# Kernel optimization log

Measured on AMD Instinct MI355X. Metric: run time of the kernel, lower is better.

Reference implementation:

```python
import jax, jax.numpy as jnp
import numpy as np

B, K, U, P, H, L, TD = 512, 1024, 16, 32, 128, 32, 64
THETA_LO, THETA_HI = 1e-3, 2.0


def _glorot(key, shape):
    fan = shape[0] + shape[1]
    lim = np.sqrt(6.0 / fan).astype(np.float32)
    return jax.random.uniform(key, shape, jnp.float32, -lim, lim)


def setup_inputs() -> dict:
    key = jax.random.key(0)
    ks = jax.random.split(key, 12)
    return {
        "y0": jax.random.normal(ks[0], (B, P), jnp.float32),
        "u_seq": jax.random.normal(ks[1], (B, K, U), jnp.float32),
        "dt_seq": jax.random.uniform(ks[2], (B, K), jnp.float32),
        "y_seq": jax.random.normal(ks[3], (B, K, P), jnp.float32),
        "u_to_y_jump": _glorot(ks[4], (U, P)),
        "lift_W": _glorot(ks[5], (L, U + P)),
        "lift_b": jnp.zeros((L,), jnp.float32),
        "w_ih": _glorot(ks[6], (3 * H, L)),
        "w_hh": _glorot(ks[7], (3 * H, H)),
        "b_ih": jnp.zeros((3 * H,), jnp.float32),
        "b_hh": jnp.zeros((3 * H,), jnp.float32),
        "head_W": _glorot(ks[8], (TD, H)),
        "head_b": jnp.zeros((TD,), jnp.float32),
        "tf_every": 50,
    }


def _rk4_step(y, h_dt, theta):
    # scaffold: linear ODE f(y) = -a*y + b, a=theta[:, :P], b=theta[:, P:]
    a, b = theta[:, :P], theta[:, P:]
    f = lambda yy: -a * yy + b
    k1 = f(y)
    k2 = f(y + 0.5 * h_dt * k1)
    k3 = f(y + 0.5 * h_dt * k2)
    k4 = f(y + h_dt * k3)
    return y + (h_dt / 6.0) * (k1 + 2.0 * k2 + 2.0 * k3 + k4)


def _forward(y0, u_seq, dt_seq, y_seq, u_to_y_jump, lift_W, lift_b,
             w_ih, w_hh, b_ih, b_hh, head_W, head_b, tf_every):
    k_idx = jnp.arange(K)
    use_tf = (k_idx > 0) & (k_idx % tf_every == 0)            # (K,)
    y_tf = jnp.concatenate([y_seq[:, :1], y_seq[:, :-1]], 1)  # y_seq[:, k-1]
    xs = (jnp.swapaxes(u_seq, 0, 1),                 # (K,B,U)
          jnp.swapaxes(dt_seq, 0, 1)[..., None],     # (K,B,1)
          jnp.swapaxes(y_tf, 0, 1),                  # (K,B,P)
          use_tf)

    def step(carry, xk):
        y_prev, h = carry
        u_k, dt_k, ytf_k, tf_k = xk
        y_in = jax.lax.stop_gradient(jnp.where(tf_k, ytf_k, y_prev))
        feat = jnp.concatenate([u_k, y_in], -1)               # (B, U+P)
        x = jax.nn.silu(feat @ lift_W.T + lift_b)             # (B, L)
        gi = x @ w_ih.T + b_ih                                # (B, 3H)
        gh = h @ w_hh.T + b_hh                                # (B, 3H)
        i_r, i_z, i_n = jnp.split(gi, 3, -1)
        h_r, h_z, h_n = jnp.split(gh, 3, -1)
        r = jax.nn.sigmoid(i_r + h_r)
        zg = jax.nn.sigmoid(i_z + h_z)
        n = jnp.tanh(i_n + r * h_n)
        h_new = (1.0 - zg) * n + zg * h                       # PyTorch GRU update
        raw = h_new @ head_W.T + head_b
        theta = THETA_LO + (THETA_HI - THETA_LO) * jax.nn.sigmoid(raw)
        y = y_prev + u_k @ u_to_y_jump                        # input jump
        y = _rk4_step(y, dt_k, theta)                         # n_substeps = 1
        return (y, h_new), (y, theta)

    h0 = jnp.zeros((y0.shape[0], H), u_seq.dtype)
    _, (ys, ths) = jax.lax.scan(step, (y0, h0), xs)
    return jnp.swapaxes(ys, 0, 1), jnp.swapaxes(ths, 0, 1)   # (B,K,P), (B,K,TD)


def reference(y0, u_seq, dt_seq, y_seq, u_to_y_jump, lift_W, lift_b,
              w_ih, w_hh, b_ih, b_hh, head_W, head_b, tf_every):
    return _forward(y0, u_seq, dt_seq, y_seq, u_to_y_jump, lift_W, lift_b,
                    w_ih, w_hh, b_ih, b_hh, head_W, head_b, tf_every)
```

## Files before the change

kernel.cpp:

```cpp
#include <hip/hip_runtime.h>
#include <math.h>


typedef float v2f __attribute__((ext_vector_type(2)));

__device__ __forceinline__ v2f mkv2(float a, float b) {
  v2f r; r.x = a; r.y = b; return r;
}

#define PKD4(acc2, v, w2, pb)                                             \
  acc2 = __builtin_elementwise_fma(mkv2((v).x, (v).y), (w2)[(pb)], acc2); \
  acc2 = __builtin_elementwise_fma(mkv2((v).z, (v).w), (w2)[(pb) + 1], acc2);

__device__ __forceinline__ float sigf(float x) {
  return 1.0f / (1.0f + __expf(-x));
}

__device__ __forceinline__ float tanh_fast(float x) {
  float ax = fabsf(x);
  float e = __expf(2.0f * ax);
  float r = 1.0f - 2.0f / (e + 1.0f);
  return copysignf(r, x);
}

template <int CTRL>
__device__ __forceinline__ float dpp_add(float x) {
  int s = __float_as_int(x);
  int r = __builtin_amdgcn_update_dpp(s, s, CTRL, 0xF, 0xF, false);
  return x + __int_as_float(r);
}

#define HP(c) ((c) + 4 * ((c) >> 5))
#define HROW 144

extern "C" __global__ __launch_bounds__(512, 2) void odernn_kernel(
    const float* __restrict__ y0, const float* __restrict__ u_seq,
    const float* __restrict__ dt_seq, const float* __restrict__ y_seq,
    const float* __restrict__ u2y, const float* __restrict__ lift_W,
    const float* __restrict__ lift_b, const float* __restrict__ w_ih,
    const float* __restrict__ w_hh, const float* __restrict__ b_ih,
    const float* __restrict__ b_hh, const float* __restrict__ head_W,
    const float* __restrict__ head_b, const int* __restrict__ tf_p,
    float* __restrict__ out_ys, float* __restrict__ out_th) {
  __shared__ __align__(16) float hbufP[2][2][HROW];
  __shared__ __align__(16) float xL[2][32];
  __shared__ __align__(16) float featL[2][48];
  __shared__ float thetaL[2][64];
  __shared__ float dtL[2];
  __shared__ float liftL[32 * 49];
  __shared__ float u2yL[512];

  const int t = threadIdx.x;
  const int b0 = blockIdx.x * 2;
  const int j = t >> 2;
  const int qj = t & 3;
  const int ho = t >> 3;
  const int he = t & 7;
  const int tfe = *tf_p;

  v2f wr2[20], wz2[20], wn2[20];
  {
    const int jr = j, jz = j + 128, jn = j + 256;
#pragma unroll
    for (int cc = 0; cc < 8; ++cc) {
      const int c = 8 * qj + cc;
      wr2[cc >> 1][cc & 1] = w_ih[jr * 32 + c];
      wz2[cc >> 1][cc & 1] = w_ih[jz * 32 + c];
      wn2[cc >> 1][cc & 1] = w_ih[jn * 32 + c];
    }
#pragma unroll
    for (int cc = 0; cc < 32; ++cc) {
      const int c = 32 * qj + cc;
      wr2[4 + (cc >> 1)][cc & 1] = w_hh[jr * 128 + c];
      wz2[4 + (cc >> 1)][cc & 1] = w_hh[jz * 128 + c];
      wn2[4 + (cc >> 1)][cc & 1] = w_hh[jn * 128 + c];
    }
  }
  v2f wh2[8];
#pragma unroll
  for (int i = 0; i < 16; ++i)
    wh2[i >> 1][i & 1] = head_W[ho * 128 + 16 * he + i];

  const float bR = b_ih[j] + b_hh[j];
  const float bZ = b_ih[j + 128] + b_hh[j + 128];
  const float bIn = b_ih[j + 256];
  const float bHn = b_hh[j + 256];
  const float hb = head_b[ho];
  const float lb = lift_b[t & 31];

  for (int idx = t; idx < 32 * 48; idx += 512)
    liftL[(idx / 48) * 49 + (idx % 48)] = lift_W[idx];
  u2yL[t] = u2y[t];
  for (int idx = t; idx < 2 * 2 * HROW; idx += 512)
    (&hbufP[0][0][0])[idx] = 0.0f;

  float hreg[2] = {0.0f, 0.0f};
  float yreg = 0.0f;
  float upf = 0.0f, dtpf = 0.0f;
  if (t < 64) yreg = y0[(b0 + (t >> 5)) * 32 + (t & 31)];

  __syncthreads();

  if (t < 64) {
    const int bb = t >> 5, jj = t & 31;
    if (t < 32)
      featL[t >> 4][t & 15] =
          u_seq[((size_t)(b0 + (t >> 4)) * 1024 + 0) * 16 + (t & 15)];
    if (t >= 32 && t < 34) dtL[t - 32] = dt_seq[(size_t)(b0 + t - 32) * 1024];
    featL[bb][16 + jj] = yreg;
    if (t < 32)
      upf = u_seq[((size_t)(b0 + (t >> 4)) * 1024 + 1) * 16 + (t & 15)];
    if (t >= 32 && t < 34) dtpf = dt_seq[(size_t)(b0 + t - 32) * 1024 + 1];
    v2f a2 = {0.f, 0.f};
#pragma unroll
    for (int i = 0; i < 48; i += 2)
      a2 = __builtin_elementwise_fma(
          mkv2(featL[bb][i], featL[bb][i + 1]),
          mkv2(liftL[jj * 49 + i], liftL[jj * 49 + i + 1]), a2);
    float acc = a2.x + a2.y + lb;
    xL[bb][jj] = acc * sigf(acc);
  }
  int mtfk = 0;
  __syncthreads();

  for (int k = 0; k < 1024; ++k) {
    const int rp = k & 1;

#pragma unroll
    for (int bb = 0; bb < 2; ++bb) {
      v2f aR2 = {0.f, 0.f}, aZ2 = {0.f, 0.f};
      v2f aI2 = {0.f, 0.f}, aN2 = {0.f, 0.f};
      const float4* xv = reinterpret_cast<const float4*>(&xL[bb][8 * qj]);
      {
        float4 v = xv[0];
        PKD4(aR2, v, wr2, 0) PKD4(aZ2, v, wz2, 0) PKD4(aI2, v, wn2, 0)
        v = xv[1];
        PKD4(aR2, v, wr2, 2) PKD4(aZ2, v, wz2, 2) PKD4(aI2, v, wn2, 2)
      }
      const float4* hv =
          reinterpret_cast<const float4*>(&hbufP[rp][bb][36 * qj]);
#pragma unroll
      for (int i = 0; i < 8; ++i) {
        float4 v = hv[i];
        PKD4(aR2, v, wr2, 4 + 2 * i)
        PKD4(aZ2, v, wz2, 4 + 2 * i)
        PKD4(aN2, v, wn2, 4 + 2 * i)
      }
      float aR = aR2.x + aR2.y;
      float aZ = aZ2.x + aZ2.y;
      float aI = aI2.x + aI2.y;
      float aN = aN2.x + aN2.y;
      aR = dpp_add<0xB1>(aR); aR = dpp_add<0x4E>(aR);
      aZ = dpp_add<0xB1>(aZ); aZ = dpp_add<0x4E>(aZ);
      aI = dpp_add<0xB1>(aI); aI = dpp_add<0x4E>(aI);
      aN = dpp_add<0xB1>(aN); aN = dpp_add<0x4E>(aN);
      float r = sigf(aR + bR);
      float z = sigf(aZ + bZ);
      float n = tanh_fast(aI + bIn + r * (aN + bHn));
      float hn = (1.0f - z) * n + z * hreg[bb];
      hreg[bb] = hn;
      if (qj == 0) hbufP[rp ^ 1][bb][HP(j)] = hn;
    }
    __syncthreads();

    {
      float s[2];
#pragma unroll
      for (int bb = 0; bb < 2; ++bb) {
        const float4* h4 =
            reinterpret_cast<const float4*>(&hbufP[rp ^ 1][bb][HP(16 * he)]);
        v2f a2 = {0.f, 0.f};
#pragma unroll
        for (int i = 0; i < 4; ++i) {
          float4 v = h4[i];
          PKD4(a2, v, wh2, 2 * i)
        }
        float a = a2.x + a2.y;
        a = dpp_add<0xB1>(a); a = dpp_add<0x4E>(a); a = dpp_add<0x104>(a);
        s[bb] = a;
      }
      if (he == 0) {
#pragma unroll
        for (int bb = 0; bb < 2; ++bb) {
          float th = 0.001f + 1.999f * sigf(s[bb] + hb);
          thetaL[bb][ho] = th;
          out_th[((size_t)(b0 + bb) * 1024 + k) * 64 + ho] = th;
        }
      }
    }
    __syncthreads();

    if (t < 64) {
      const int bb = t >> 5, jj = t & 31;
      v2f y2 = {0.f, 0.f};
#pragma unroll
      for (int i = 0; i < 16; i += 2)
        y2 = __builtin_elementwise_fma(
            mkv2(featL[bb][i], featL[bb][i + 1]),
            mkv2(u2yL[i * 32 + jj], u2yL[(i + 1) * 32 + jj]), y2);
      float y = yreg + y2.x + y2.y;
      float a = thetaL[bb][jj];
      float b2 = thetaL[bb][32 + jj];
      float hdt = dtL[bb];
      float k1 = b2 - a * y;
      float k2 = b2 - a * (y + 0.5f * hdt * k1);
      float k3 = b2 - a * (y + 0.5f * hdt * k2);
      float k4 = b2 - a * (y + hdt * k3);
      y += hdt * (1.0f / 6.0f) * (k1 + 2.0f * k2 + 2.0f * k3 + k4);
      yreg = y;
      out_ys[((size_t)(b0 + bb) * 1024 + k) * 32 + jj] = y;
      if (t < 32) featL[t >> 4][t & 15] = upf;
      if (t >= 32 && t < 34) dtL[t - 32] = dtpf;
      {
        const int kn = (k + 2 < 1024) ? k + 2 : 1023;
        if (t < 32)
          upf = u_seq[((size_t)(b0 + (t >> 4)) * 1024 + kn) * 16 + (t & 15)];
        if (t >= 32 && t < 34)
          dtpf = dt_seq[(size_t)(b0 + t - 32) * 1024 + kn];
      }
      float yin = y;
      if (mtfk == tfe - 1)
        yin = y_seq[((size_t)(b0 + bb) * 1024 + k) * 32 + jj];
      featL[bb][16 + jj] = yin;
      v2f a2 = {0.f, 0.f};
#pragma unroll
      for (int i = 0; i < 48; i += 2)
        a2 = __builtin_elementwise_fma(
            mkv2(featL[bb][i], featL[bb][i + 1]),
            mkv2(liftL[jj * 49 + i], liftL[jj * 49 + i + 1]), a2);
      float acc = a2.x + a2.y + lb;
      xL[bb][jj] = acc * sigf(acc);
    }
    mtfk = (mtfk + 1 == tfe) ? 0 : mtfk + 1;
    __syncthreads();
  }
}

extern "C" void kernel_launch(void* const* d_in, const int* in_sizes, int n_in,
                              void* d_out, int out_size, void* d_ws,
                              size_t ws_size, hipStream_t stream) {
  (void)in_sizes; (void)n_in; (void)out_size; (void)d_ws; (void)ws_size;
  const float* y0     = (const float*)d_in[0];
  const float* u_seq  = (const float*)d_in[1];
  const float* dt_seq = (const float*)d_in[2];
  const float* y_seq  = (const float*)d_in[3];
  const float* u2y    = (const float*)d_in[4];
  const float* lift_W = (const float*)d_in[5];
  const float* lift_b = (const float*)d_in[6];
  const float* w_ih   = (const float*)d_in[7];
  const float* w_hh   = (const float*)d_in[8];
  const float* b_ih   = (const float*)d_in[9];
  const float* b_hh   = (const float*)d_in[10];
  const float* head_W = (const float*)d_in[11];
  const float* head_b = (const float*)d_in[12];
  const int*   tf_p   = (const int*)d_in[13];

  float* out_ys = (float*)d_out;
  float* out_th = out_ys + (size_t)512 * 1024 * 32;

  odernn_kernel<<<dim3(256), dim3(512), 0, stream>>>(
      y0, u_seq, dt_seq, y_seq, u2y, lift_W, lift_b, w_ih, w_hh, b_ih, b_hh,
      head_W, head_b, tf_p, out_ys, out_th);
}
```

Baseline: 2.751 ms.

## Replicate lift/RK4 stage per wavefront to drop a block barrier per step

Every wavefront now redundantly computes the input jump, RK4 update and lift MLP into its own private shared-memory copies of feat, x and dt. Each wave reads only its own copy in the next GRU step, so the third block-wide barrier per timestep is removed. The remaining barriers use a hand-rolled s_waitcnt lgkmcnt(0) plus s_barrier instead of __syncthreads. The cost is eight times the work on this small stage and more redundant global prefetch loads, in exchange for one fewer full-block sync on the serial critical path.

Measured after the change: 3.049 ms. 1.11x slower.

```diff
diff --git a/kernel.cpp b/kernel.cpp
--- a/kernel.cpp
+++ b/kernel.cpp
@@ -29,6 +29,13 @@
   int r = __builtin_amdgcn_update_dpp(s, s, CTRL, 0xF, 0xF, false);
   return x + __int_as_float(r);
 }
+
+#define BAR()                                            \
+  do {                                                   \
+    asm volatile("s_waitcnt lgkmcnt(0)" ::: "memory");   \
+    __builtin_amdgcn_s_barrier();                        \
+    asm volatile("" ::: "memory");                       \
+  } while (0)
 
 #define HP(c) ((c) + 4 * ((c) >> 5))
 #define HROW 144
@@ -43,14 +50,16 @@
     const float* __restrict__ head_b, const int* __restrict__ tf_p,
     float* __restrict__ out_ys, float* __restrict__ out_th) {
   __shared__ __align__(16) float hbufP[2][2][HROW];
-  __shared__ __align__(16) float xL[2][32];
-  __shared__ __align__(16) float featL[2][48];
+  __shared__ __align__(16) float xW[8][2][32];
+  __shared__ __align__(16) float featW[8][2][48];
+  __shared__ float dtW[8][2];
   __shared__ float thetaL[2][64];
-  __shared__ float dtL[2];
   __shared__ float liftL[32 * 49];
   __shared__ float u2yL[512];
 
   const int t = threadIdx.x;
+  const int wv = t >> 6;
+  const int l = t & 63;
   const int b0 = blockIdx.x * 2;
   const int j = t >> 2;
   const int qj = t & 3;
@@ -86,7 +95,7 @@
   const float bIn = b_ih[j + 256];
   const float bHn = b_hh[j + 256];
   const float hb = head_b[ho];
-  const float lb = lift_b[t & 31];
+  const float lb = lift_b[l & 31];
 
   for (int idx = t; idx < 32 * 48; idx += 512)
     liftL[(idx / 48) * 49 + (idx % 48)] = lift_W[idx];
@@ -95,30 +104,26 @@
     (&hbufP[0][0][0])[idx] = 0.0f;
 
   float hreg[2] = {0.0f, 0.0f};
-  float yreg = 0.0f;
+  float yreg = y0[(b0 + (l >> 5)) * 32 + (l & 31)];
   float upf = 0.0f, dtpf = 0.0f;
-  if (t < 64) yreg = y0[(b0 + (t >> 5)) * 32 + (t & 31)];
-
-  __syncthreads();
-
-  if (t < 64) {
-    const int bb = t >> 5, jj = t & 31;
-    if (t < 32)
-      featL[t >> 4][t & 15] =
-          u_seq[((size_t)(b0 + (t >> 4)) * 1024 + 0) * 16 + (t & 15)];
-    if (t >= 32 && t < 34) dtL[t - 32] = dt_seq[(size_t)(b0 + t - 32) * 1024];
-    featL[bb][16 + jj] = yreg;
-    if (t < 32)
-      upf = u_seq[((size_t)(b0 + (t >> 4)) * 1024 + 1) * 16 + (t & 15)];
-    if (t >= 32 && t < 34) dtpf = dt_seq[(size_t)(b0 + t - 32) * 1024 + 1];
+  if (l < 32) upf = u_seq[((size_t)(b0 + (l >> 4)) * 1024 + 1) * 16 + (l & 15)];
+  if (l >= 32 && l < 34) dtpf = dt_seq[(size_t)(b0 + l - 32) * 1024 + 1];
+
+  {
+    const int bb = l >> 5, jj = l & 31;
+    if (l < 32)
+      featW[wv][l >> 4][l & 15] =
+          u_seq[((size_t)(b0 + (l >> 4)) * 1024 + 0) * 16 + (l & 15)];
+    if (l >= 32 && l < 34) dtW[wv][l - 32] = dt_seq[(size_t)(b0 + l - 32) * 1024];
+    featW[wv][bb][16 + jj] = yreg;
     v2f a2 = {0.f, 0.f};
 #pragma unroll
     for (int i = 0; i < 48; i += 2)
       a2 = __builtin_elementwise_fma(
-          mkv2(featL[bb][i], featL[bb][i + 1]),
+          mkv2(featW[wv][bb][i], featW[wv][bb][i + 1]),
           mkv2(liftL[jj * 49 + i], liftL[jj * 49 + i + 1]), a2);
     float acc = a2.x + a2.y + lb;
-    xL[bb][jj] = acc * sigf(acc);
+    xW[wv][bb][jj] = acc * sigf(acc);
   }
   int mtfk = 0;
   __syncthreads();
@@ -130,7 +135,7 @@
     for (int bb = 0; bb < 2; ++bb) {
       v2f aR2 = {0.f, 0.f}, aZ2 = {0.f, 0.f};
       v2f aI2 = {0.f, 0.f}, aN2 = {0.f, 0.f};
-      const float4* xv = reinterpret_cast<const float4*>(&xL[bb][8 * qj]);
+      const float4* xv = reinterpret_cast<const float4*>(&xW[wv][bb][8 * qj]);
       {
         float4 v = xv[0];
         PKD4(aR2, v, wr2, 0) PKD4(aZ2, v, wz2, 0) PKD4(aI2, v, wn2, 0)
@@ -161,7 +166,7 @@
       hreg[bb] = hn;
       if (qj == 0) hbufP[rp ^ 1][bb][HP(j)] = hn;
     }
-    __syncthreads();
+    BAR();
 
     {
       float s[2];
@@ -188,51 +193,50 @@
         }
       }
     }
-    __syncthreads();
-
-    if (t < 64) {
-      const int bb = t >> 5, jj = t & 31;
+    BAR();
+
+    {
+      const int bb = l >> 5, jj = l & 31;
       v2f y2 = {0.f, 0.f};
 #pragma unroll
       for (int i = 0; i < 16; i += 2)
         y2 = __builtin_elementwise_fma(
-            mkv2(featL[bb][i], featL[bb][i + 1]),
+            mkv2(featW[wv][bb][i], featW[wv][bb][i + 1]),
             mkv2(u2yL[i * 32 + jj], u2yL[(i + 1) * 32 + jj]), y2);
       float y = yreg + y2.x + y2.y;
       float a = thetaL[bb][jj];
       float b2 = thetaL[bb][32 + jj];
-      float hdt = dtL[bb];
+      float hdt = dtW[wv][bb];
       float k1 = b2 - a * y;
       float k2 = b2 - a * (y + 0.5f * hdt * k1);
       float k3 = b2 - a * (y + 0.5f * hdt * k2);
       float k4 = b2 - a * (y + hdt * k3);
       y += hdt * (1.0f / 6.0f) * (k1 + 2.0f * k2 + 2.0f * k3 + k4);
       yreg = y;
-      out_ys[((size_t)(b0 + bb) * 1024 + k) * 32 + jj] = y;
-      if (t < 32) featL[t >> 4][t & 15] = upf;
-      if (t >= 32 && t < 34) dtL[t - 32] = dtpf;
+      if (wv == 0) out_ys[((size_t)(b0 + bb) * 1024 + k) * 32 + jj] = y;
+      if (l < 32) featW[wv][l >> 4][l & 15] = upf;
+      if (l >= 32 && l < 34) dtW[wv][l - 32] = dtpf;
       {
         const int kn = (k + 2 < 1024) ? k + 2 : 1023;
-        if (t < 32)
-          upf = u_seq[((size_t)(b0 + (t >> 4)) * 1024 + kn) * 16 + (t & 15)];
-        if (t >= 32 && t < 34)
-          dtpf = dt_seq[(size_t)(b0 + t - 32) * 1024 + kn];
+        if (l < 32)
+          upf = u_seq[((size_t)(b0 + (l >> 4)) * 1024 + kn) * 16 + (l & 15)];
+        if (l >= 32 && l < 34)
+          dtpf = dt_seq[(size_t)(b0 + l - 32) * 1024 + kn];
       }
       float yin = y;
       if (mtfk == tfe - 1)
         yin = y_seq[((size_t)(b0 + bb) * 1024 + k) * 32 + jj];
-      featL[bb][16 + jj] = yin;
+      featW[wv][bb][16 + jj] = yin;
       v2f a2 = {0.f, 0.f};
 #pragma unroll
       for (int i = 0; i < 48; i += 2)
         a2 = __builtin_elementwise_fma(
-            mkv2(featL[bb][i], featL[bb][i + 1]),
+            mkv2(featW[wv][bb][i], featW[wv][bb][i + 1]),
             mkv2(liftL[jj * 49 + i], liftL[jj * 49 + i + 1]), a2);
       float acc = a2.x + a2.y + lb;
-      xL[bb][jj] = acc * sigf(acc);
+      xW[wv][bb][jj] = acc * sigf(acc);
     }
     mtfk = (mtfk + 1 == tfe) ? 0 : mtfk + 1;
-    __syncthreads();
   }
 }
 
```
